# Kernel optimization log

Hardware: AMD Instinct MI355X
Metric: run time of the kernel (lower is better)

## Reference

```python
import jax, jax.numpy as jnp
import numpy as np

B = 262144   # batch of candidate user-item pairs
D = 256      # concat embedding dim (embedding_dim*8)
H = 128      # hypernet hidden
HD = 32      # expert hidden dim
E = 4        # num experts


def setup_inputs() -> dict:
    key = jax.random.key(0)
    ks = jax.random.split(key, 16)
    def w(k, shape, fan_in):
        return jax.random.normal(k, shape, jnp.float32) * (1.0 / np.sqrt(fan_in))
    return {
        "x": jax.random.normal(ks[0], (B, D), jnp.float32),
        "context_embed": jax.random.normal(ks[1], (D,), jnp.float32),
        # hypernet (soft_module_route)
        "W1": w(ks[2], (D, H), D),   "b1": jnp.zeros((H,), jnp.float32),
        "W2": w(ks[3], (H, H), H),   "b2": jnp.zeros((H,), jnp.float32),
        "W12": w(ks[4], (H, E * E), H), "b12": jnp.zeros((E * E,), jnp.float32),
        "W22": w(ks[5], (H, E), H),     "b22": jnp.zeros((E,), jnp.float32),
        # soft_module experts: stacked per-expert Linear weights
        "Wf1": w(ks[6], (E, D, HD), D), "bf1": jnp.zeros((E, HD), jnp.float32),
        "Wf2": w(ks[7], (E, HD, HD), HD), "bf2": jnp.zeros((E, HD), jnp.float32),
        "Wfin": w(ks[8], (HD, 1), HD),  "bfin": jnp.zeros((1,), jnp.float32),
    }


def reference(x, context_embed, W1, b1, W2, b2, W12, b12, W22, b22,
              Wf1, bf1, Wf2, bf2, Wfin, bfin):
    # hypernet: routing weights from x * context
    embeds = x * context_embed[None, :]                       # [B,D]
    h = jax.nn.relu(embeds @ W1 + b1)                         # [B,H]
    c1 = jax.nn.softmax((h @ W12 + b12).reshape(-1, E, E), axis=1)   # [B,4,4]
    h2 = jax.nn.relu(h @ W2 + b2)                             # [B,H]
    c2 = jax.nn.softmax((h2 @ W22 + b22).reshape(-1, E, 1), axis=1)  # [B,4,1]
    # soft_module: 4 experts per layer, soft combined via c1/c2
    o1 = jax.nn.relu(jnp.einsum('bd,edh->bhe', x, Wf1) + bf1.T)      # [B,HD,E]
    in2 = jnp.einsum('bhe,bef->bhf', o1, c1)                         # [B,HD,E]
    o2 = jax.nn.relu(jnp.einsum('bhe,ehk->bke', in2, Wf2) + bf2.T)   # [B,HD,E]
    in3 = jnp.einsum('bke,bef->bkf', o2, c2)[..., 0]                 # [B,HD]
    return in3 @ Wfin + bfin                                         # [B,1]
```

## Files before the change

### kernel.cpp

```cpp
#include <hip/hip_runtime.h>
#include <hip/hip_bf16.h>

typedef _Float16 f16;
typedef _Float16 half8 __attribute__((ext_vector_type(8)));
typedef _Float16 half4 __attribute__((ext_vector_type(4)));
typedef float floatx4 __attribute__((ext_vector_type(4)));

#define BM 64

#define WA_OFF 0
#define WB_OFF 65536
#define WC_OFF 83968
#define WF2_OFF 86016
#define WSF_BYTE_OFF 180224
#define BA_OFF 0
#define BB_OFF 256
#define BCC_OFF 400
#define BF2_OFF 404
#define WFIN_OFF 532
#define BFIN_OFF 564

__global__ __launch_bounds__(256) void prep_kernel(
    const float* __restrict__ ctx, const float* __restrict__ W1,
    const float* __restrict__ b1, const float* __restrict__ W2,
    const float* __restrict__ b2, const float* __restrict__ W12,
    const float* __restrict__ b12, const float* __restrict__ W22,
    const float* __restrict__ b22, const float* __restrict__ Wf1,
    const float* __restrict__ bf1, const float* __restrict__ Wf2,
    const float* __restrict__ bf2, const float* __restrict__ Wfin,
    const float* __restrict__ bfin, f16* __restrict__ wsh,
    float* __restrict__ wsf)
{
  int tid = blockIdx.x * 256 + threadIdx.x;
  if (tid < 65536) {
    int j = tid & 7, l = (tid >> 3) & 63, kt = (tid >> 9) & 7, nt = tid >> 12;
    int k = kt * 32 + ((l >> 4) << 3) + j, n = nt * 16 + (l & 15);
    float v;
    if (n < 128) v = ctx[k] * W1[k * 128 + n];
    else { int c = n - 128; v = Wf1[((c >> 5) * 256 + k) * 32 + (c & 31)]; }
    wsh[tid] = (f16)v;
  } else if (tid < WB_OFF + 18432) {
    int o = tid - WB_OFF;
    int j = o & 7, l = (o >> 3) & 63, kt = (o >> 9) & 3, nt = o >> 11;
    int k = kt * 32 + ((l >> 4) << 3) + j, n = nt * 16 + (l & 15);
    float v = (n < 128) ? W2[k * 128 + n] : W12[k * 16 + (n - 128)];
    wsh[tid] = (f16)v;
  } else if (tid < WC_OFF + 2048) {
    int o = tid - WC_OFF;
    int j = o & 7, l = (o >> 3) & 63, kt = (o >> 9) & 3;
    int k = kt * 32 + ((l >> 4) << 3) + j, n = l & 15;
    float v = (n < 4) ? W22[k * 4 + n] : 0.f;
    wsh[tid] = (f16)v;
  } else if (tid < WF2_OFF + 4096) {
    int o = tid - WF2_OFF;
    int j = o & 7, l = (o >> 3) & 63, ent = o >> 9;
    int e = ent >> 1, nt = ent & 1;
    int k = ((l >> 4) << 3) + j, n = nt * 16 + (l & 15);
    wsh[tid] = (f16)Wf2[(e * 32 + k) * 32 + n];
  } else if (tid < 90112 + 565) {
    int o = tid - 90112;
    float v;
    if (o < 128) v = b1[o];
    else if (o < 256) v = bf1[o - 128];
    else if (o < 384) v = b2[o - 256];
    else if (o < 400) v = b12[o - 384];
    else if (o < 404) v = b22[o - 400];
    else if (o < 532) v = bf2[o - 404];
    else if (o < 564) v = Wfin[o - 532];
    else v = bfin[0];
    wsf[o] = v;
  }
}

#define MFMA16(A, Bv, C) __builtin_amdgcn_mfma_f32_16x16x32_f16(A, Bv, C, 0, 0, 0)

#define G_OFF 0
#define H2_OFF 32768
#define L1_OFF 49152
#define PART_OFF 49152
#define L2_OFF 51200
#define C2_OFF 52224

__global__ __launch_bounds__(256, 3) void fused_kernel(
    const float* __restrict__ x, const f16* __restrict__ wsh,
    const float* __restrict__ wsf, float* __restrict__ out)
{
  __shared__ __attribute__((aligned(16))) char lds[53248];
  const int t = threadIdx.x;
  const int lane = t & 63;
  const int w = t >> 6;
  const int l15 = lane & 15;
  const int l4 = lane >> 4;
  const size_t base = (size_t)blockIdx.x * BM;

#pragma unroll
  for (int it = 0; it < 8; ++it) {
    int c = it * 256 + t;
    int r = c >> 5;
    int k0 = (c & 31) << 3;
    const float4* xv = (const float4*)(x + (base + (size_t)r) * 256 + k0);
    float4 a = xv[0], b = xv[1];
    half8 hv;
    hv[0] = (f16)a.x; hv[1] = (f16)a.y; hv[2] = (f16)a.z; hv[3] = (f16)a.w;
    hv[4] = (f16)b.x; hv[5] = (f16)b.y; hv[6] = (f16)b.z; hv[7] = (f16)b.w;
    int addr = (r * 512 + k0 * 2) ^ ((r & 7) << 4);
    *(half8*)(lds + addr) = hv;
  }
  __syncthreads();

  floatx4 acc[4][4];
#pragma unroll
  for (int q = 0; q < 4; ++q)
#pragma unroll
    for (int mt = 0; mt < 4; ++mt) acc[q][mt] = (floatx4){0.f, 0.f, 0.f, 0.f};
  for (int kt = 0; kt < 8; ++kt) {
    half8 Bx[4];
#pragma unroll
    for (int mt = 0; mt < 4; ++mt) {
      int r = mt * 16 + l15;
      int addr = (r * 512 + kt * 64 + (l4 << 4)) ^ ((r & 7) << 4);
      Bx[mt] = *(const half8*)(lds + addr);
    }
#pragma unroll
    for (int q = 0; q < 4; ++q) {
      half8 Wf = *(const half8*)(wsh + WA_OFF + (size_t)(((w * 4 + q) * 8 + kt) * 64 + lane) * 8);
#pragma unroll
      for (int mt = 0; mt < 4; ++mt) acc[q][mt] = MFMA16(Wf, Bx[mt], acc[q][mt]);
    }
  }
  __syncthreads();
#pragma unroll
  for (int q = 0; q < 4; ++q) {
    int c0 = (w * 4 + q) * 16 + l4 * 4;
    float4 bias = *(const float4*)(wsf + BA_OFF + c0);
#pragma unroll
    for (int mt = 0; mt < 4; ++mt) {
      int r = mt * 16 + l15;
      half4 hv;
#pragma unroll
      for (int i = 0; i < 4; ++i) hv[i] = (f16)fmaxf(acc[q][mt][i] + ((const float*)&bias)[i], 0.f);
      int addr = (r * 512 + c0 * 2) ^ ((r & 7) << 4);
      *(half4*)(lds + addr) = hv;
    }
  }
  __syncthreads();

  {
    floatx4 acc2[2][4];
    floatx4 accL[4];
#pragma unroll
    for (int qi = 0; qi < 2; ++qi)
#pragma unroll
      for (int mt = 0; mt < 4; ++mt) acc2[qi][mt] = (floatx4){0.f, 0.f, 0.f, 0.f};
#pragma unroll
    for (int mt = 0; mt < 4; ++mt) accL[mt] = (floatx4){0.f, 0.f, 0.f, 0.f};

    for (int kt = 0; kt < 4; ++kt) {
      half8 Bh[4];
#pragma unroll
      for (int mt = 0; mt < 4; ++mt) {
        int r = mt * 16 + l15;
        int addr = (r * 512 + kt * 64 + (l4 << 4)) ^ ((r & 7) << 4);
        Bh[mt] = *(const half8*)(lds + addr);
      }
#pragma unroll
      for (int qi = 0; qi < 2; ++qi) {
        half8 Wf = *(const half8*)(wsh + WB_OFF + (size_t)(((w + qi * 4) * 4 + kt) * 64 + lane) * 8);
#pragma unroll
        for (int mt = 0; mt < 4; ++mt) acc2[qi][mt] = MFMA16(Wf, Bh[mt], acc2[qi][mt]);
      }
      if (w == 3) {
        half8 Wf = *(const half8*)(wsh + WB_OFF + (size_t)((32 + kt) * 64 + lane) * 8);
#pragma unroll
        for (int mt = 0; mt < 4; ++mt) accL[mt] = MFMA16(Wf, Bh[mt], accL[mt]);
      }
    }
#pragma unroll
    for (int qi = 0; qi < 2; ++qi) {
      int c0 = (w + qi * 4) * 16 + l4 * 4;
      float4 bias = *(const float4*)(wsf + BB_OFF + c0);
#pragma unroll
      for (int mt = 0; mt < 4; ++mt) {
        int r = mt * 16 + l15;
        half4 hv;
#pragma unroll
        for (int i = 0; i < 4; ++i) hv[i] = (f16)fmaxf(acc2[qi][mt][i] + ((const float*)&bias)[i], 0.f);
        int addr = H2_OFF + ((r * 256 + c0 * 2) ^ ((r & 7) << 4));
        *(half4*)(lds + addr) = hv;
      }
    }
    if (w == 3) {
      int c0 = l4 * 4;
      float4 bias = *(const float4*)(wsf + BB_OFF + 128 + c0);
#pragma unroll
      for (int mt = 0; mt < 4; ++mt) {
        int r = mt * 16 + l15;
        half4 hv;
#pragma unroll
        for (int i = 0; i < 4; ++i) hv[i] = (f16)(accL[mt][i] + ((const float*)&bias)[i]);
        *(half4*)(lds + L1_OFF + r * 32 + c0 * 2) = hv;
      }
    }
  }
  __syncthreads();

  {
    floatx4 acc3 = (floatx4){0.f, 0.f, 0.f, 0.f};
    int r = w * 16 + l15;
#pragma unroll
    for (int kt = 0; kt < 4; ++kt) {
      int addr = H2_OFF + ((r * 256 + kt * 64 + (l4 << 4)) ^ ((r & 7) << 4));
      half8 Bh2 = *(const half8*)(lds + addr);
      half8 Wf = *(const half8*)(wsh + WC_OFF + (size_t)(kt * 64 + lane) * 8);
      acc3 = MFMA16(Wf, Bh2, acc3);
    }
    if (lane < 16) {
      float4 bias = *(const float4*)(wsf + BCC_OFF);
      float4 v;
      v.x = acc3[0] + bias.x; v.y = acc3[1] + bias.y;
      v.z = acc3[2] + bias.z; v.w = acc3[3] + bias.w;
      *(float4*)(lds + L2_OFF + (w * 16 + lane) * 16) = v;
    }
  }
  __syncthreads();

  {
    int r = t >> 2, f = t & 3;
    const f16* L1p = (const f16*)(lds + L1_OFF) + r * 16 + f;
    float a0 = (float)L1p[0], a1 = (float)L1p[4], a2 = (float)L1p[8], a3 = (float)L1p[12];
    float m = fmaxf(fmaxf(a0, a1), fmaxf(a2, a3));
    float e0 = __expf(a0 - m), e1 = __expf(a1 - m), e2 = __expf(a2 - m), e3 = __expf(a3 - m);
    float inv = 1.f / (e0 + e1 + e2 + e3);
    float c0v = e0 * inv, c1v = e1 * inv, c2v = e2 * inv, c3v = e3 * inv;
    int sw = (r & 7) << 4;
#pragma unroll
    for (int h8 = 0; h8 < 4; ++h8) {
      half8 o0 = *(const half8*)(lds + ((r * 512 + 256 + 0   + h8 * 16) ^ sw));
      half8 o1v = *(const half8*)(lds + ((r * 512 + 256 + 64  + h8 * 16) ^ sw));
      half8 o2v = *(const half8*)(lds + ((r * 512 + 256 + 128 + h8 * 16) ^ sw));
      half8 o3v = *(const half8*)(lds + ((r * 512 + 256 + 192 + h8 * 16) ^ sw));
      half8 res;
#pragma unroll
      for (int j = 0; j < 8; ++j) {
        float v = c0v * (float)o0[j] + c1v * (float)o1v[j] + c2v * (float)o2v[j] + c3v * (float)o3v[j];
        res[j] = (f16)v;
      }
      *(half8*)(lds + H2_OFF + ((r * 256 + f * 64 + h8 * 16) ^ sw)) = res;
    }
    if (f == 0) {
      float4 q = *(const float4*)(lds + L2_OFF + r * 16);
      float m2 = fmaxf(fmaxf(q.x, q.y), fmaxf(q.z, q.w));
      float f0 = __expf(q.x - m2), f1 = __expf(q.y - m2), f2 = __expf(q.z - m2), f3 = __expf(q.w - m2);
      float inv2 = 1.f / (f0 + f1 + f2 + f3);
      float4 c2o; c2o.x = f0 * inv2; c2o.y = f1 * inv2; c2o.z = f2 * inv2; c2o.w = f3 * inv2;
      *(float4*)(lds + C2_OFF + r * 16) = c2o;
    }
  }
  __syncthreads();

  {
    floatx4 acc4[2][4];
#pragma unroll
    for (int ct = 0; ct < 2; ++ct)
#pragma unroll
      for (int mt = 0; mt < 4; ++mt) acc4[ct][mt] = (floatx4){0.f, 0.f, 0.f, 0.f};
    half8 Bi[4];
#pragma unroll
    for (int mt = 0; mt < 4; ++mt) {
      int r = mt * 16 + l15;
      int addr = H2_OFF + ((r * 256 + w * 64 + (l4 << 4)) ^ ((r & 7) << 4));
      Bi[mt] = *(const half8*)(lds + addr);
    }
#pragma unroll
    for (int ct = 0; ct < 2; ++ct) {
      half8 Wf = *(const half8*)(wsh + WF2_OFF + (size_t)((w * 2 + ct) * 64 + lane) * 8);
#pragma unroll
      for (int mt = 0; mt < 4; ++mt) acc4[ct][mt] = MFMA16(Wf, Bi[mt], acc4[ct][mt]);
    }
    float4 bias0 = *(const float4*)(wsf + BF2_OFF + w * 32 + l4 * 4);
    float4 bias1 = *(const float4*)(wsf + BF2_OFF + w * 32 + 16 + l4 * 4);
    float4 wf0 = *(const float4*)(wsf + WFIN_OFF + l4 * 4);
    float4 wf1 = *(const float4*)(wsf + WFIN_OFF + 16 + l4 * 4);
#pragma unroll
    for (int mt = 0; mt < 4; ++mt) {
      int r = mt * 16 + l15;
      float s = 0.f;
#pragma unroll
      for (int i = 0; i < 4; ++i) {
        s += fmaxf(acc4[0][mt][i] + ((const float*)&bias0)[i], 0.f) * ((const float*)&wf0)[i];
        s += fmaxf(acc4[1][mt][i] + ((const float*)&bias1)[i], 0.f) * ((const float*)&wf1)[i];
      }
      s += __shfl_xor(s, 16);
      s += __shfl_xor(s, 32);
      if (l4 == 0) {
        float c2e = *(const float*)(lds + C2_OFF + r * 16 + w * 4);
        *(float*)(lds + PART_OFF + (w * 64 + r) * 4) = s * c2e;
      }
    }
  }
  __syncthreads();

  if (t < 64) {
    float s = wsf[BFIN_OFF];
#pragma unroll
    for (int e = 0; e < 4; ++e) s += *(const float*)(lds + PART_OFF + e * 256 + t * 4);
    out[base + t] = s;
  }
}

extern "C" void kernel_launch(void* const* d_in, const int* in_sizes, int n_in,
                              void* d_out, int out_size, void* d_ws, size_t ws_size,
                              hipStream_t stream) {
  (void)in_sizes; (void)n_in; (void)ws_size;
  const float* x    = (const float*)d_in[0];
  const float* ctx  = (const float*)d_in[1];
  const float* W1   = (const float*)d_in[2];
  const float* b1   = (const float*)d_in[3];
  const float* W2   = (const float*)d_in[4];
  const float* b2   = (const float*)d_in[5];
  const float* W12  = (const float*)d_in[6];
  const float* b12  = (const float*)d_in[7];
  const float* W22  = (const float*)d_in[8];
  const float* b22  = (const float*)d_in[9];
  const float* Wf1  = (const float*)d_in[10];
  const float* bf1  = (const float*)d_in[11];
  const float* Wf2  = (const float*)d_in[12];
  const float* bf2  = (const float*)d_in[13];
  const float* Wfin = (const float*)d_in[14];
  const float* bfin = (const float*)d_in[15];

  f16* wsh = (f16*)d_ws;
  float* wsf = (float*)((char*)d_ws + WSF_BYTE_OFF);

  prep_kernel<<<355, 256, 0, stream>>>(ctx, W1, b1, W2, b2, W12, b12, W22, b22,
                                       Wf1, bf1, Wf2, bf2, Wfin, bfin, wsh, wsf);

  int nblocks = 262144 / BM;
  fused_kernel<<<nblocks, 256, 0, stream>>>(x, wsh, wsf, (float*)d_out);
}
```

Measured before the change: 102.4 us.

## Alias LDS buffers to cut shared memory and raise occupancy to four blocks

```diff
diff --git a/kernel.cpp b/kernel.cpp
--- a/kernel.cpp
+++ b/kernel.cpp
@@ -74,18 +74,15 @@
 
 #define MFMA16(A, Bv, C) __builtin_amdgcn_mfma_f32_16x16x32_f16(A, Bv, C, 0, 0, 0)
 
-#define G_OFF 0
-#define H2_OFF 32768
-#define L1_OFF 49152
-#define PART_OFF 49152
-#define L2_OFF 51200
-#define C2_OFF 52224
-
-__global__ __launch_bounds__(256, 3) void fused_kernel(
+#define L1_OFF 32768
+#define PART_OFF 32768
+#define C2_OFF 34816
+
+__global__ __launch_bounds__(256, 4) void fused_kernel(
     const float* __restrict__ x, const f16* __restrict__ wsh,
     const float* __restrict__ wsf, float* __restrict__ out)
 {
-  __shared__ __attribute__((aligned(16))) char lds[53248];
+  __shared__ __attribute__((aligned(16))) char lds[35840];
   const int t = threadIdx.x;
   const int lane = t & 63;
   const int w = t >> 6;
@@ -108,39 +105,41 @@
   }
   __syncthreads();
 
-  floatx4 acc[4][4];
-#pragma unroll
-  for (int q = 0; q < 4; ++q)
-#pragma unroll
-    for (int mt = 0; mt < 4; ++mt) acc[q][mt] = (floatx4){0.f, 0.f, 0.f, 0.f};
-  for (int kt = 0; kt < 8; ++kt) {
-    half8 Bx[4];
-#pragma unroll
-    for (int mt = 0; mt < 4; ++mt) {
-      int r = mt * 16 + l15;
-      int addr = (r * 512 + kt * 64 + (l4 << 4)) ^ ((r & 7) << 4);
-      Bx[mt] = *(const half8*)(lds + addr);
-    }
+  {
+    floatx4 acc[4][4];
+#pragma unroll
+    for (int q = 0; q < 4; ++q)
+#pragma unroll
+      for (int mt = 0; mt < 4; ++mt) acc[q][mt] = (floatx4){0.f, 0.f, 0.f, 0.f};
+    for (int kt = 0; kt < 8; ++kt) {
+      half8 Bx[4];
+#pragma unroll
+      for (int mt = 0; mt < 4; ++mt) {
+        int r = mt * 16 + l15;
+        int addr = (r * 512 + kt * 64 + (l4 << 4)) ^ ((r & 7) << 4);
+        Bx[mt] = *(const half8*)(lds + addr);
+      }
+#pragma unroll
+      for (int q = 0; q < 4; ++q) {
+        half8 Wf = *(const half8*)(wsh + WA_OFF + (size_t)(((w * 4 + q) * 8 + kt) * 64 + lane) * 8);
+#pragma unroll
+        for (int mt = 0; mt < 4; ++mt) acc[q][mt] = MFMA16(Wf, Bx[mt], acc[q][mt]);
+      }
+    }
+    __syncthreads();
 #pragma unroll
     for (int q = 0; q < 4; ++q) {
-      half8 Wf = *(const half8*)(wsh + WA_OFF + (size_t)(((w * 4 + q) * 8 + kt) * 64 + lane) * 8);
-#pragma unroll
-      for (int mt = 0; mt < 4; ++mt) acc[q][mt] = MFMA16(Wf, Bx[mt], acc[q][mt]);
-    }
-  }
-  __syncthreads();
-#pragma unroll
-  for (int q = 0; q < 4; ++q) {
-    int c0 = (w * 4 + q) * 16 + l4 * 4;
-    float4 bias = *(const float4*)(wsf + BA_OFF + c0);
-#pragma unroll
-    for (int mt = 0; mt < 4; ++mt) {
-      int r = mt * 16 + l15;
-      half4 hv;
-#pragma unroll
-      for (int i = 0; i < 4; ++i) hv[i] = (f16)fmaxf(acc[q][mt][i] + ((const float*)&bias)[i], 0.f);
-      int addr = (r * 512 + c0 * 2) ^ ((r & 7) << 4);
-      *(half4*)(lds + addr) = hv;
+      int c0 = (w * 4 + q) * 16 + l4 * 4;
+      float4 bias = *(const float4*)(wsf + BA_OFF + c0);
+#pragma unroll
+      for (int mt = 0; mt < 4; ++mt) {
+        int r = mt * 16 + l15;
+        half4 hv;
+#pragma unroll
+        for (int i = 0; i < 4; ++i) hv[i] = (f16)fmaxf(acc[q][mt][i] + ((const float*)&bias)[i], 0.f);
+        int addr = (r * 512 + c0 * 2) ^ ((r & 7) << 4);
+        *(half4*)(lds + addr) = hv;
+      }
     }
   }
   __syncthreads();
@@ -175,6 +174,7 @@
         for (int mt = 0; mt < 4; ++mt) accL[mt] = MFMA16(Wf, Bh[mt], accL[mt]);
       }
     }
+    __syncthreads();
 #pragma unroll
     for (int qi = 0; qi < 2; ++qi) {
       int c0 = (w + qi * 4) * 16 + l4 * 4;
@@ -185,7 +185,7 @@
         half4 hv;
 #pragma unroll
         for (int i = 0; i < 4; ++i) hv[i] = (f16)fmaxf(acc2[qi][mt][i] + ((const float*)&bias)[i], 0.f);
-        int addr = H2_OFF + ((r * 256 + c0 * 2) ^ ((r & 7) << 4));
+        int addr = (r * 512 + c0 * 2) ^ ((r & 7) << 4);
         *(half4*)(lds + addr) = hv;
       }
     }
@@ -209,20 +209,24 @@
     int r = w * 16 + l15;
 #pragma unroll
     for (int kt = 0; kt < 4; ++kt) {
-      int addr = H2_OFF + ((r * 256 + kt * 64 + (l4 << 4)) ^ ((r & 7) << 4));
+      int addr = (r * 512 + kt * 64 + (l4 << 4)) ^ ((r & 7) << 4);
       half8 Bh2 = *(const half8*)(lds + addr);
       half8 Wf = *(const half8*)(wsh + WC_OFF + (size_t)(kt * 64 + lane) * 8);
       acc3 = MFMA16(Wf, Bh2, acc3);
     }
     if (lane < 16) {
       float4 bias = *(const float4*)(wsf + BCC_OFF);
-      float4 v;
-      v.x = acc3[0] + bias.x; v.y = acc3[1] + bias.y;
-      v.z = acc3[2] + bias.z; v.w = acc3[3] + bias.w;
-      *(float4*)(lds + L2_OFF + (w * 16 + lane) * 16) = v;
-    }
-  }
-  __syncthreads();
+      float q0 = acc3[0] + bias.x, q1 = acc3[1] + bias.y;
+      float q2 = acc3[2] + bias.z, q3 = acc3[3] + bias.w;
+      float m2 = fmaxf(fmaxf(q0, q1), fmaxf(q2, q3));
+      float f0 = __expf(q0 - m2), f1 = __expf(q1 - m2);
+      float f2 = __expf(q2 - m2), f3 = __expf(q3 - m2);
+      float inv2 = 1.f / (f0 + f1 + f2 + f3);
+      float4 c2o;
+      c2o.x = f0 * inv2; c2o.y = f1 * inv2; c2o.z = f2 * inv2; c2o.w = f3 * inv2;
+      *(float4*)(lds + C2_OFF + r * 16) = c2o;
+    }
+  }
 
   {
     int r = t >> 2, f = t & 3;
@@ -233,28 +237,25 @@
     float inv = 1.f / (e0 + e1 + e2 + e3);
     float c0v = e0 * inv, c1v = e1 * inv, c2v = e2 * inv, c3v = e3 * inv;
     int sw = (r & 7) << 4;
+    half8 res[4];
 #pragma unroll
     for (int h8 = 0; h8 < 4; ++h8) {
       half8 o0 = *(const half8*)(lds + ((r * 512 + 256 + 0   + h8 * 16) ^ sw));
       half8 o1v = *(const half8*)(lds + ((r * 512 + 256 + 64  + h8 * 16) ^ sw));
       half8 o2v = *(const half8*)(lds + ((r * 512 + 256 + 128 + h8 * 16) ^ sw));
       half8 o3v = *(const half8*)(lds + ((r * 512 + 256 + 192 + h8 * 16) ^ sw));
-      half8 res;
+      half8 rr;
 #pragma unroll
       for (int j = 0; j < 8; ++j) {
         float v = c0v * (float)o0[j] + c1v * (float)o1v[j] + c2v * (float)o2v[j] + c3v * (float)o3v[j];
-        res[j] = (f16)v;
-      }
-      *(half8*)(lds + H2_OFF + ((r * 256 + f * 64 + h8 * 16) ^ sw)) = res;
-    }
-    if (f == 0) {
-      float4 q = *(const float4*)(lds + L2_OFF + r * 16);
-      float m2 = fmaxf(fmaxf(q.x, q.y), fmaxf(q.z, q.w));
-      float f0 = __expf(q.x - m2), f1 = __expf(q.y - m2), f2 = __expf(q.z - m2), f3 = __expf(q.w - m2);
-      float inv2 = 1.f / (f0 + f1 + f2 + f3);
-      float4 c2o; c2o.x = f0 * inv2; c2o.y = f1 * inv2; c2o.z = f2 * inv2; c2o.w = f3 * inv2;
-      *(float4*)(lds + C2_OFF + r * 16) = c2o;
-    }
+        rr[j] = (f16)v;
+      }
+      res[h8] = rr;
+    }
+    __syncthreads();
+#pragma unroll
+    for (int h8 = 0; h8 < 4; ++h8)
+      *(half8*)(lds + ((r * 512 + 256 + f * 64 + h8 * 16) ^ sw)) = res[h8];
   }
   __syncthreads();
 
@@ -268,7 +269,7 @@
 #pragma unroll
     for (int mt = 0; mt < 4; ++mt) {
       int r = mt * 16 + l15;
-      int addr = H2_OFF + ((r * 256 + w * 64 + (l4 << 4)) ^ ((r & 7) << 4));
+      int addr = (r * 512 + 256 + w * 64 + (l4 << 4)) ^ ((r & 7) << 4);
       Bi[mt] = *(const half8*)(lds + addr);
     }
 #pragma unroll
```

Result: slower. 114.9 us (+12.2%).
